# Performance work log

Hardware: AMD Instinct MI355X
Metric: run time of the kernel (lower is better)

The kernel has to match this reference:

```python
import jax, jax.numpy as jnp
import numpy as np

B, C, H, W = 4, 512, 64, 64
C8 = C // 8


def setup_inputs() -> dict:
    key = jax.random.key(0)
    ks = jax.random.split(key, 12)
    s = lambda fan_in: 1.0 / np.sqrt(fan_in)
    return {
        "final_encoded": jax.random.normal(ks[0], (B, C, H, W), jnp.float32),
        "total": jax.random.normal(ks[1], (B, C, H, W), jnp.float32),
        # 1x1 conv weights (out, in) and biases
        "Wq": jax.random.normal(ks[2], (C8, C), jnp.float32) * s(C),
        "bq": jax.random.normal(ks[3], (C8,), jnp.float32) * s(C),
        "Wk": jax.random.normal(ks[4], (C8, C), jnp.float32) * s(C),
        "bk": jax.random.normal(ks[5], (C8,), jnp.float32) * s(C),
        "Wv": jax.random.normal(ks[6], (C, C), jnp.float32) * s(C),
        "bv": jax.random.normal(ks[7], (C,), jnp.float32) * s(C),
        # learned additive positional tensors
        "height_tensor": jax.random.normal(ks[8], (1, C8, H, 1), jnp.float32),
        "width_tensor": jax.random.normal(ks[9], (1, C8, 1, W), jnp.float32),
        "gamma": jnp.zeros((1,), jnp.float32),
    }


def reference(final_encoded, total, Wq, bq, Wk, bk, Wv, bv, height_tensor, width_tensor, gamma):
    b, c, h, w = final_encoded.shape
    c8 = c // 8
    hw = h * w
    # 1x1 convs as channel matmuls
    q = jnp.einsum("oc,bchw->bohw", Wq, total) + bq[None, :, None, None]
    k = jnp.einsum("oc,bchw->bohw", Wk, final_encoded) + bk[None, :, None, None]
    v = jnp.einsum("oc,bchw->bohw", Wv, final_encoded) + bv[None, :, None, None]
    pq = q.reshape(b, c8, hw).transpose(0, 2, 1)   # [B, HW, C8]
    pk = k.reshape(b, c8, hw)                      # [B, C8, HW]
    pv = v.reshape(b, c, hw)                       # [B, C, HW]
    energy = jnp.einsum("bnc,bcm->bnm", pq, pk)    # [B, HW, HW] content energy
    pos = (height_tensor + width_tensor).reshape(c8, hw)  # [C8, HW] additive positional bias basis
    energy = energy + jnp.einsum("bnc,cm->bnm", pq, pos)
    attention = jax.nn.softmax(energy, axis=-1)
    # out = bmm(value, attention^T)
    out = jnp.einsum("bcm,bnm->bcn", pv, attention).reshape(b, c, h, w)
    return gamma * out + final_encoded
```

## Files before the change

### kernel.cpp

```cpp
#include <hip/hip_runtime.h>
#include <hip/hip_bf16.h>

#define B_   4
#define C_   512
#define C8_  64
#define HW_  4096

typedef short bf16x8 __attribute__((ext_vector_type(8)));
typedef float f32x4  __attribute__((ext_vector_type(4)));

__device__ __forceinline__ unsigned short f2bf(float f) {
  union { unsigned int i; float f; } x; x.f = f;
  unsigned int r = x.i + 0x7fffu + ((x.i >> 16) & 1u);
  return (unsigned short)(r >> 16);
}

__device__ __forceinline__ unsigned int cvtpk(float lo, float hi) {
  unsigned int r;
  asm("v_cvt_pk_bf16_f32 %0, %1, %2" : "=v"(r) : "v"(lo), "v"(hi));
  return r;
}

__device__ __forceinline__ float fexp2(float x) {
  float r;
  asm("v_exp_f32 %0, %1" : "=v"(r) : "v"(x));
  return r;
}

#define MFMA(a, b, c) __builtin_amdgcn_mfma_f32_16x16x32_bf16((a), (b), (c), 0, 0, 0)

#define LOG2E 1.44269504f
#define NEG20LOG2E -28.8539008f


__global__ __launch_bounds__(640) void proj_kernel(
    const float* __restrict__ total, const float* __restrict__ fe,
    const float* __restrict__ Wq, const float* __restrict__ bq,
    const float* __restrict__ Wk, const float* __restrict__ bk,
    const float* __restrict__ Wv, const float* __restrict__ bv,
    const float* __restrict__ ht, const float* __restrict__ wt,
    unsigned short* __restrict__ Qh, unsigned short* __restrict__ Kh,
    unsigned short* __restrict__ Vn) {
  __shared__ __align__(16) unsigned short Ws[640 * 72];
  __shared__ __align__(16) unsigned short Xf[64 * 72];
  __shared__ __align__(16) unsigned short Xt[64 * 72];

  const int t = threadIdx.x;
  const int b = blockIdx.y;
  const int x = blockIdx.x;
  const int m0 = x * 64;
  const int lane = t & 63, w = t >> 6, ln = lane & 15, quad = lane >> 4;

  const int c4 = t & 15;
  const int orow = t >> 4;

  f32x4 acc[4][4];
#pragma unroll
  for (int ct = 0; ct < 4; ++ct)
#pragma unroll
    for (int mt = 0; mt < 4; ++mt) acc[ct][mt] = f32x4{0.f, 0.f, 0.f, 0.f};

  for (int kb = 0; kb < 8; ++kb) {
    const int c0 = kb * 64;
#pragma unroll
    for (int i = 0; i < 16; ++i) {
      const int o = i * 40 + orow;
      const float* src = (o < 64) ? &Wq[(size_t)o * C_]
                       : (o < 128) ? &Wk[(size_t)(o - 64) * C_]
                                   : &Wv[(size_t)(o - 128) * C_];
      f32x4 wv = *(const f32x4*)&src[c0 + c4 * 4];
      *(uint2*)&Ws[o * 72 + c4 * 4] =
          make_uint2(cvtpk(wv[0], wv[1]), cvtpk(wv[2], wv[3]));
    }
    if (t < 512) {
      const int t2 = t & 255;
      const float* Xsrc = (t < 256) ? fe : total;
      unsigned short* Xdst = (t < 256) ? Xf : Xt;
      const int rc4 = t2 >> 4, mq = t2 & 15;
      f32x4 xv[4];
#pragma unroll
      for (int k = 0; k < 4; ++k)
        xv[k] = *(const f32x4*)&Xsrc[((size_t)b * C_ + c0 + rc4 * 4 + k) * HW_ + m0 + mq * 4];
#pragma unroll
      for (int j = 0; j < 4; ++j)
        *(uint2*)&Xdst[(mq * 4 + j) * 72 + rc4 * 4] =
            make_uint2(cvtpk(xv[0][j], xv[1][j]), cvtpk(xv[2][j], xv[3][j]));
    }
    __syncthreads();
    const unsigned short* Xsel = (w == 0) ? Xt : Xf;
    bf16x8 aw[4][2], bx[4][2];
#pragma unroll
    for (int ct = 0; ct < 4; ++ct) {
      aw[ct][0] = *(const bf16x8*)&Ws[(w * 64 + ct * 16 + ln) * 72 + quad * 8];
      aw[ct][1] = *(const bf16x8*)&Ws[(w * 64 + ct * 16 + ln) * 72 + 32 + quad * 8];
    }
#pragma unroll
    for (int mt = 0; mt < 4; ++mt) {
      bx[mt][0] = *(const bf16x8*)&Xsel[(mt * 16 + ln) * 72 + quad * 8];
      bx[mt][1] = *(const bf16x8*)&Xsel[(mt * 16 + ln) * 72 + 32 + quad * 8];
    }
#pragma unroll
    for (int ct = 0; ct < 4; ++ct)
#pragma unroll
      for (int mt = 0; mt < 4; ++mt) {
        acc[ct][mt] = MFMA(aw[ct][0], bx[mt][0], acc[ct][mt]);
        acc[ct][mt] = MFMA(aw[ct][1], bx[mt][1], acc[ct][mt]);
      }
    __syncthreads();
  }

  if (w == 0) {
#pragma unroll
    for (int ct = 0; ct < 4; ++ct)
#pragma unroll
      for (int mt = 0; mt < 4; ++mt)
#pragma unroll
        for (int r = 0; r < 4; ++r) {
          const int o = ct * 16 + quad * 4 + r;
          const float val = (acc[ct][mt][r] + bq[o]) * LOG2E;
          const size_t idx = ((size_t)b * 512 + (x * 4 + mt) * 2 + (ct >> 1)) * 512
                           + ((((ct & 1) << 1) | (quad >> 1))) * 128
                           + ln * 8 + ((quad & 1) << 2) + r;
          Qh[idx] = f2bf(val);
        }
  } else if (w == 1) {
#pragma unroll
    for (int ct = 0; ct < 4; ++ct)
#pragma unroll
      for (int mt = 0; mt < 4; ++mt)
#pragma unroll
        for (int r = 0; r < 4; ++r) {
          const int o = ct * 16 + quad * 4 + r;
          const float val = acc[ct][mt][r] + bk[o] + ht[o * 64 + x] + wt[o * 64 + mt * 16 + ln];
          const size_t idx = ((size_t)b * 512 + (x * 4 + mt) * 2 + (ct >> 1)) * 512
                           + ((((ct & 1) << 1) | (quad >> 1))) * 128
                           + ln * 8 + ((quad & 1) << 2) + r;
          Kh[idx] = f2bf(val);
        }
  } else {
#pragma unroll
    for (int ct = 0; ct < 4; ++ct) {
      const int cht = w * 4 - 8 + ct;
#pragma unroll
      for (int r = 0; r < 4; ++r) {
        const float bz = bv[cht * 16 + quad * 4 + r];
#pragma unroll
        for (int mt = 0; mt < 4; ++mt) {
          const size_t idx = (((size_t)b * 32 + cht) * 128 + (size_t)x * 2 + (mt >> 1)) * 512
                           + (((mt & 1) * 2) + (ln >> 3)) * 128 + (quad * 4 + r) * 8 + (ln & 7);
          Vn[idx] = f2bf(acc[ct][mt][r] + bz);
        }
      }
    }
  }
}

__global__ __launch_bounds__(512, 4) void flash_kernel(
    const unsigned short* __restrict__ Qh, const unsigned short* __restrict__ Kh,
    const unsigned short* __restrict__ Vn, const float* __restrict__ fe,
    const float* __restrict__ gamma, float* __restrict__ out) {
  __shared__ __align__(16) unsigned short Ps[2][64 * 64];
  __shared__ float Red[2][64];

  const int t = threadIdx.x;
  const int n = blockIdx.x;
  const int xcd = n & 7;
  const int b = xcd & 3;
  const int ch0 = (xcd >> 2) * 256;
  const int q0 = (n >> 3) * 64;
  const int lane = t & 63, w = t >> 6, ln = lane & 15, quad = lane >> 4;
  const int qt = w & 3;
  const int kh = w >> 2;
  const int swz = (ln & 7) << 4;

  const unsigned short* Qb = Qh + (size_t)b * 512 * 512;
  const unsigned short* Kb = Kh + (size_t)b * 512 * 512;
  const unsigned short* Vbase = Vn + ((size_t)b * 32 + (ch0 >> 4)) * (128 * 512);

  const bf16x8 aq0 = *(const bf16x8*)&Qb[((size_t)((q0 >> 4) + qt) * 2 + 0) * 512 + lane * 8];
  const bf16x8 aq1 = *(const bf16x8*)&Qb[((size_t)((q0 >> 4) + qt) * 2 + 1) * 512 + lane * 8];

  const f32x4 CINIT = {NEG20LOG2E, NEG20LOG2E, NEG20LOG2E, NEG20LOG2E};

  float Sacc = 0.f;
  f32x4 acc[2][4];
#pragma unroll
  for (int mt = 0; mt < 2; ++mt)
#pragma unroll
    for (int nt = 0; nt < 4; ++nt) acc[mt][nt] = f32x4{0.f, 0.f, 0.f, 0.f};

  bf16x8 kf[2][2];
  bf16x8 vf[2][2];

  auto loadK = [&](int it) {
#pragma unroll
    for (int nt = 0; nt < 2; ++nt)
#pragma unroll
      for (int hf = 0; hf < 2; ++hf)
        kf[nt][hf] = *(const bf16x8*)&Kb[((size_t)(it * 4 + kh * 2 + nt) * 2 + hf) * 512 + lane * 8];
  };
  auto loadV = [&](int it) {
#pragma unroll
    for (int mt = 0; mt < 2; ++mt)
#pragma unroll
      for (int kc = 0; kc < 2; ++kc)
        vf[mt][kc] = *(const bf16x8*)&Vbase[(((size_t)(w * 2 + mt)) * 128 + it * 2 + kc) * 512 + lane * 8];
  };

  const int qrow = qt * 16 + ln;

  auto writeP = [&](f32x4 e0, f32x4 e1, char* Pw) {
    const float p0 = fexp2(e0[0]), p1 = fexp2(e0[1]);
    const float p2 = fexp2(e0[2]), p3 = fexp2(e0[3]);
    Sacc += (p0 + p1) + (p2 + p3);
    *(uint2*)(Pw + ((qrow * 128 + kh * 64 + quad * 8) ^ swz)) =
        make_uint2(cvtpk(p0, p1), cvtpk(p2, p3));
    const float s0 = fexp2(e1[0]), s1 = fexp2(e1[1]);
    const float s2 = fexp2(e1[2]), s3 = fexp2(e1[3]);
    Sacc += (s0 + s1) + (s2 + s3);
    *(uint2*)(Pw + ((qrow * 128 + kh * 64 + 32 + quad * 8) ^ swz)) =
        make_uint2(cvtpk(s0, s1), cvtpk(s2, s3));
  };

  loadK(0);
  loadV(0);

  {
    f32x4 e0 = MFMA(kf[0][0], aq0, CINIT);
    e0 = MFMA(kf[0][1], aq1, e0);
    f32x4 e1 = MFMA(kf[1][0], aq0, CINIT);
    e1 = MFMA(kf[1][1], aq1, e1);
    writeP(e0, e1, (char*)Ps[0]);
  }
  loadK(1);
  asm volatile("s_waitcnt lgkmcnt(0)" ::: "memory");
  __builtin_amdgcn_s_barrier();
  asm volatile("" ::: "memory");

  for (int it = 0; it < 64; ++it) {
    char* Prd = (char*)Ps[it & 1];
    char* Pwr = (char*)Ps[(it + 1) & 1];
    bf16x8 bp0[4];
#pragma unroll
    for (int nt = 0; nt < 4; ++nt)
      bp0[nt] = *(const bf16x8*)(Prd + ((((nt * 16 + ln) * 128 + quad * 16)) ^ swz));
    if (it < 63) {
      __builtin_amdgcn_s_setprio(1);
      f32x4 e0 = MFMA(kf[0][0], aq0, CINIT);
      e0 = MFMA(kf[0][1], aq1, e0);
      f32x4 e1 = MFMA(kf[1][0], aq0, CINIT);
      e1 = MFMA(kf[1][1], aq1, e1);
      __builtin_amdgcn_s_setprio(0);
      if (it < 62) loadK(it + 2);
      writeP(e0, e1, Pwr);
    }
    __builtin_amdgcn_s_setprio(1);
#pragma unroll
    for (int mt = 0; mt < 2; ++mt)
#pragma unroll
      for (int nt = 0; nt < 4; ++nt)
        acc[mt][nt] = MFMA(vf[mt][0], bp0[nt], acc[mt][nt]);
    __builtin_amdgcn_s_setprio(0);
    bf16x8 bp1[4];
#pragma unroll
    for (int nt = 0; nt < 4; ++nt)
      bp1[nt] = *(const bf16x8*)(Prd + ((((nt * 16 + ln) * 128 + 64 + quad * 16)) ^ swz));
    __builtin_amdgcn_s_setprio(1);
#pragma unroll
    for (int mt = 0; mt < 2; ++mt)
#pragma unroll
      for (int nt = 0; nt < 4; ++nt)
        acc[mt][nt] = MFMA(vf[mt][1], bp1[nt], acc[mt][nt]);
    __builtin_amdgcn_s_setprio(0);
    if (it < 63) {
      loadV(it + 1);
      asm volatile("s_waitcnt lgkmcnt(0)" ::: "memory");
      __builtin_amdgcn_s_barrier();
      asm volatile("" ::: "memory");
    }
  }

  {
    float s = Sacc;
    s += __shfl_xor(s, 16);
    s += __shfl_xor(s, 32);
    if (quad == 0) Red[kh][qrow] = s;
  }
  __syncthreads();
  float rsv[4];
#pragma unroll
  for (int nt = 0; nt < 4; ++nt)
    rsv[nt] = 1.0f / (Red[0][nt * 16 + ln] + Red[1][nt * 16 + ln]);

  const float g = gamma[0];
#pragma unroll
  for (int mt = 0; mt < 2; ++mt) {
#pragma unroll
    for (int r = 0; r < 4; ++r) {
      const int ch = ch0 + w * 32 + mt * 16 + quad * 4 + r;
      const size_t base = ((size_t)b * C_ + ch) * HW_ + q0;
#pragma unroll
      for (int nt = 0; nt < 4; ++nt) {
        const size_t idx = base + nt * 16 + ln;
        out[idx] = g * (acc[mt][nt][r] * rsv[nt]) + fe[idx];
      }
    }
  }
}

extern "C" void kernel_launch(void* const* d_in, const int* in_sizes, int n_in,
                              void* d_out, int out_size, void* d_ws, size_t ws_size,
                              hipStream_t stream) {
  const float* fe    = (const float*)d_in[0];
  const float* total = (const float*)d_in[1];
  const float* Wq    = (const float*)d_in[2];
  const float* bq    = (const float*)d_in[3];
  const float* Wk    = (const float*)d_in[4];
  const float* bk    = (const float*)d_in[5];
  const float* Wv    = (const float*)d_in[6];
  const float* bv    = (const float*)d_in[7];
  const float* ht    = (const float*)d_in[8];
  const float* wt    = (const float*)d_in[9];
  const float* gamma = (const float*)d_in[10];
  float* out = (float*)d_out;

  unsigned short* Qh = (unsigned short*)d_ws;
  unsigned short* Kh = Qh + (size_t)B_ * HW_ * C8_;
  unsigned short* Vn = Kh + (size_t)B_ * HW_ * C8_;

  proj_kernel<<<dim3(64, B_), 640, 0, stream>>>(total, fe, Wq, bq, Wk, bk,
                                                Wv, bv, ht, wt, Qh, Kh, Vn);
  flash_kernel<<<dim3(512), 512, 0, stream>>>(Qh, Kh, Vn, fe, gamma, out);
}
```

Before: 231.8 us.

## Double query tile per block to 128 rows to halve K/V reloads

Each flash block now handles 128 query rows instead of 64. Every wave computes two 16-row query subtiles against the same K fragments, and the PV accumulators grow to 8 column tiles. The grid is halved to 256 blocks, so each loaded K and V fragment is reused across twice as many queries and global traffic for K/V drops. In exchange, register pressure rises (launch bounds lowered to 2 blocks), the LDS P buffer doubles, and 256 blocks may underfill the CUs of an MI355X.

```diff
diff --git a/kernel.cpp b/kernel.cpp
--- a/kernel.cpp
+++ b/kernel.cpp
@@ -155,21 +155,21 @@
   }
 }
 
-__global__ __launch_bounds__(512, 4) void flash_kernel(
+__global__ __launch_bounds__(512, 2) void flash_kernel(
     const unsigned short* __restrict__ Qh, const unsigned short* __restrict__ Kh,
     const unsigned short* __restrict__ Vn, const float* __restrict__ fe,
     const float* __restrict__ gamma, float* __restrict__ out) {
-  __shared__ __align__(16) unsigned short Ps[2][64 * 64];
-  __shared__ float Red[2][64];
+  __shared__ __align__(16) unsigned short Ps[2][128 * 64];
+  __shared__ float Red[2][128];
 
   const int t = threadIdx.x;
   const int n = blockIdx.x;
   const int xcd = n & 7;
   const int b = xcd & 3;
   const int ch0 = (xcd >> 2) * 256;
-  const int q0 = (n >> 3) * 64;
+  const int q0 = (n >> 3) * 128;
   const int lane = t & 63, w = t >> 6, ln = lane & 15, quad = lane >> 4;
-  const int qt = w & 3;
+  const int qs = w & 3;
   const int kh = w >> 2;
   const int swz = (ln & 7) << 4;
 
@@ -177,17 +177,22 @@
   const unsigned short* Kb = Kh + (size_t)b * 512 * 512;
   const unsigned short* Vbase = Vn + ((size_t)b * 32 + (ch0 >> 4)) * (128 * 512);
 
-  const bf16x8 aq0 = *(const bf16x8*)&Qb[((size_t)((q0 >> 4) + qt) * 2 + 0) * 512 + lane * 8];
-  const bf16x8 aq1 = *(const bf16x8*)&Qb[((size_t)((q0 >> 4) + qt) * 2 + 1) * 512 + lane * 8];
+  bf16x8 aq[2][2];
+#pragma unroll
+  for (int sub = 0; sub < 2; ++sub)
+#pragma unroll
+    for (int hf = 0; hf < 2; ++hf)
+      aq[sub][hf] = *(const bf16x8*)
+          &Qb[((size_t)((q0 >> 4) + qs * 2 + sub) * 2 + hf) * 512 + lane * 8];
 
   const f32x4 CINIT = {NEG20LOG2E, NEG20LOG2E, NEG20LOG2E, NEG20LOG2E};
 
-  float Sacc = 0.f;
-  f32x4 acc[2][4];
+  float Sacc0 = 0.f, Sacc1 = 0.f;
+  f32x4 acc[2][8];
 #pragma unroll
   for (int mt = 0; mt < 2; ++mt)
 #pragma unroll
-    for (int nt = 0; nt < 4; ++nt) acc[mt][nt] = f32x4{0.f, 0.f, 0.f, 0.f};
+    for (int nt = 0; nt < 8; ++nt) acc[mt][nt] = f32x4{0.f, 0.f, 0.f, 0.f};
 
   bf16x8 kf[2][2];
   bf16x8 vf[2][2];
@@ -207,31 +212,38 @@
         vf[mt][kc] = *(const bf16x8*)&Vbase[(((size_t)(w * 2 + mt)) * 128 + it * 2 + kc) * 512 + lane * 8];
   };
 
-  const int qrow = qt * 16 + ln;
-
-  auto writeP = [&](f32x4 e0, f32x4 e1, char* Pw) {
-    const float p0 = fexp2(e0[0]), p1 = fexp2(e0[1]);
-    const float p2 = fexp2(e0[2]), p3 = fexp2(e0[3]);
-    Sacc += (p0 + p1) + (p2 + p3);
-    *(uint2*)(Pw + ((qrow * 128 + kh * 64 + quad * 8) ^ swz)) =
-        make_uint2(cvtpk(p0, p1), cvtpk(p2, p3));
-    const float s0 = fexp2(e1[0]), s1 = fexp2(e1[1]);
-    const float s2 = fexp2(e1[2]), s3 = fexp2(e1[3]);
-    Sacc += (s0 + s1) + (s2 + s3);
-    *(uint2*)(Pw + ((qrow * 128 + kh * 64 + 32 + quad * 8) ^ swz)) =
-        make_uint2(cvtpk(s0, s1), cvtpk(s2, s3));
+  const int qr0 = qs * 32 + ln;
+
+  auto qkWrite = [&](char* Pw) {
+    f32x4 e00 = MFMA(kf[0][0], aq[0][0], CINIT);
+    e00 = MFMA(kf[0][1], aq[0][1], e00);
+    f32x4 e01 = MFMA(kf[1][0], aq[0][0], CINIT);
+    e01 = MFMA(kf[1][1], aq[0][1], e01);
+    f32x4 e10 = MFMA(kf[0][0], aq[1][0], CINIT);
+    e10 = MFMA(kf[0][1], aq[1][1], e10);
+    f32x4 e11 = MFMA(kf[1][0], aq[1][0], CINIT);
+    e11 = MFMA(kf[1][1], aq[1][1], e11);
+#pragma unroll
+    for (int kn = 0; kn < 2; ++kn) {
+      const f32x4 ea = (kn == 0) ? e00 : e01;
+      const float a0 = fexp2(ea[0]), a1 = fexp2(ea[1]);
+      const float a2 = fexp2(ea[2]), a3 = fexp2(ea[3]);
+      Sacc0 += (a0 + a1) + (a2 + a3);
+      *(uint2*)(Pw + ((qr0 * 128 + kh * 64 + kn * 32 + quad * 8) ^ swz)) =
+          make_uint2(cvtpk(a0, a1), cvtpk(a2, a3));
+      const f32x4 eb = (kn == 0) ? e10 : e11;
+      const float b0 = fexp2(eb[0]), b1 = fexp2(eb[1]);
+      const float b2 = fexp2(eb[2]), b3 = fexp2(eb[3]);
+      Sacc1 += (b0 + b1) + (b2 + b3);
+      *(uint2*)(Pw + (((qr0 + 16) * 128 + kh * 64 + kn * 32 + quad * 8) ^ swz)) =
+          make_uint2(cvtpk(b0, b1), cvtpk(b2, b3));
+    }
   };
 
   loadK(0);
   loadV(0);
 
-  {
-    f32x4 e0 = MFMA(kf[0][0], aq0, CINIT);
-    e0 = MFMA(kf[0][1], aq1, e0);
-    f32x4 e1 = MFMA(kf[1][0], aq0, CINIT);
-    e1 = MFMA(kf[1][1], aq1, e1);
-    writeP(e0, e1, (char*)Ps[0]);
-  }
+  qkWrite((char*)Ps[0]);
   loadK(1);
   asm volatile("s_waitcnt lgkmcnt(0)" ::: "memory");
   __builtin_amdgcn_s_barrier();
@@ -240,37 +252,32 @@
   for (int it = 0; it < 64; ++it) {
     char* Prd = (char*)Ps[it & 1];
     char* Pwr = (char*)Ps[(it + 1) & 1];
-    bf16x8 bp0[4];
-#pragma unroll
-    for (int nt = 0; nt < 4; ++nt)
-      bp0[nt] = *(const bf16x8*)(Prd + ((((nt * 16 + ln) * 128 + quad * 16)) ^ swz));
+    bf16x8 bp[8];
+#pragma unroll
+    for (int nt = 0; nt < 8; ++nt)
+      bp[nt] = *(const bf16x8*)(Prd + ((((nt * 16 + ln) * 128 + quad * 16)) ^ swz));
     if (it < 63) {
       __builtin_amdgcn_s_setprio(1);
-      f32x4 e0 = MFMA(kf[0][0], aq0, CINIT);
-      e0 = MFMA(kf[0][1], aq1, e0);
-      f32x4 e1 = MFMA(kf[1][0], aq0, CINIT);
-      e1 = MFMA(kf[1][1], aq1, e1);
+      qkWrite(Pwr);
       __builtin_amdgcn_s_setprio(0);
       if (it < 62) loadK(it + 2);
-      writeP(e0, e1, Pwr);
     }
     __builtin_amdgcn_s_setprio(1);
 #pragma unroll
     for (int mt = 0; mt < 2; ++mt)
 #pragma unroll
-      for (int nt = 0; nt < 4; ++nt)
-        acc[mt][nt] = MFMA(vf[mt][0], bp0[nt], acc[mt][nt]);
+      for (int nt = 0; nt < 8; ++nt)
+        acc[mt][nt] = MFMA(vf[mt][0], bp[nt], acc[mt][nt]);
     __builtin_amdgcn_s_setprio(0);
-    bf16x8 bp1[4];
-#pragma unroll
-    for (int nt = 0; nt < 4; ++nt)
-      bp1[nt] = *(const bf16x8*)(Prd + ((((nt * 16 + ln) * 128 + 64 + quad * 16)) ^ swz));
+#pragma unroll
+    for (int nt = 0; nt < 8; ++nt)
+      bp[nt] = *(const bf16x8*)(Prd + ((((nt * 16 + ln) * 128 + 64 + quad * 16)) ^ swz));
     __builtin_amdgcn_s_setprio(1);
 #pragma unroll
     for (int mt = 0; mt < 2; ++mt)
 #pragma unroll
-      for (int nt = 0; nt < 4; ++nt)
-        acc[mt][nt] = MFMA(vf[mt][1], bp1[nt], acc[mt][nt]);
+      for (int nt = 0; nt < 8; ++nt)
+        acc[mt][nt] = MFMA(vf[mt][1], bp[nt], acc[mt][nt]);
     __builtin_amdgcn_s_setprio(0);
     if (it < 63) {
       loadV(it + 1);
@@ -281,15 +288,19 @@
   }
 
   {
-    float s = Sacc;
+    float s = Sacc0;
     s += __shfl_xor(s, 16);
     s += __shfl_xor(s, 32);
-    if (quad == 0) Red[kh][qrow] = s;
+    if (quad == 0) Red[kh][qr0] = s;
+    float s1 = Sacc1;
+    s1 += __shfl_xor(s1, 16);
+    s1 += __shfl_xor(s1, 32);
+    if (quad == 0) Red[kh][qr0 + 16] = s1;
   }
   __syncthreads();
-  float rsv[4];
-#pragma unroll
-  for (int nt = 0; nt < 4; ++nt)
+  float rsv[8];
+#pragma unroll
+  for (int nt = 0; nt < 8; ++nt)
     rsv[nt] = 1.0f / (Red[0][nt * 16 + ln] + Red[1][nt * 16 + ln]);
 
   const float g = gamma[0];
@@ -300,7 +311,7 @@
       const int ch = ch0 + w * 32 + mt * 16 + quad * 4 + r;
       const size_t base = ((size_t)b * C_ + ch) * HW_ + q0;
 #pragma unroll
-      for (int nt = 0; nt < 4; ++nt) {
+      for (int nt = 0; nt < 8; ++nt) {
         const size_t idx = base + nt * 16 + ln;
         out[idx] = g * (acc[mt][nt][r] * rsv[nt]) + fe[idx];
       }
@@ -330,5 +341,5 @@
 
   proj_kernel<<<dim3(64, B_), 640, 0, stream>>>(total, fe, Wq, bq, Wk, bk,
                                                 Wv, bv, ht, wt, Qh, Kh, Vn);
-  flash_kernel<<<dim3(512), 512, 0, stream>>>(Qh, Kh, Vn, fe, gamma, out);
-}
+  flash_kernel<<<dim3(256), 512, 0, stream>>>(Qh, Kh, Vn, fe, gamma, out);
+}
```

Result: faster. 221.7 us (-4.4%).
